# Optimization experiments

Hardware: AMD Instinct MI355X
Metric: run time of the kernel (lower is better)

Reference implementation:

```python
import jax, jax.numpy as jnp
import numpy as np

H = 16  # num_heads

def _toroidal_bias(S, dtype):
    # float mask: +1.0 at (i, (i-1)%S), (i,i), (i, (i+1)%S); PyTorch ADDS float attn_mask to scores
    eye = jnp.eye(S, dtype=dtype)
    return eye + jnp.roll(eye, 1, axis=1) + jnp.roll(eye, -1, axis=1)

def setup_inputs() -> dict:
    key = jax.random.key(0)
    ks = jax.random.split(key, 7)
    E = 1024
    S, B = 2048, 2
    sc = 0.02
    return {
        "x": jax.random.normal(ks[0], (S, B, E), dtype=jnp.float32),
        "w_tor": jax.random.normal(ks[1], (E, E), dtype=jnp.float32) * sc,
        "b_tor": jax.random.normal(ks[2], (E,), dtype=jnp.float32) * sc,
        "in_proj_w": jax.random.normal(ks[3], (3 * E, E), dtype=jnp.float32) * sc,
        "in_proj_b": jax.random.normal(ks[4], (3 * E,), dtype=jnp.float32) * sc,
        "out_w": jax.random.normal(ks[5], (E, E), dtype=jnp.float32) * sc,
        "out_b": jax.random.normal(ks[6], (E,), dtype=jnp.float32) * sc,
    }

def reference(x, w_tor, b_tor, in_proj_w, in_proj_b, out_w, out_b):
    S, B, E = x.shape
    hd = E // H
    scale = 1.0 / jnp.sqrt(jnp.asarray(hd, dtype=x.dtype))
    # toroidal projection, then fused in_proj (self-attention: q=k=v=x_toroidal)
    xt = x @ w_tor.T + b_tor                      # (S,B,E)
    qkv = xt @ in_proj_w.T + in_proj_b            # (S,B,3E)
    q, k, v = jnp.split(qkv, 3, axis=-1)
    def to_heads(t):
        return t.reshape(S, B, H, hd).transpose(1, 2, 0, 3)  # (B,H,S,hd)
    q, k, v = to_heads(q), to_heads(k), to_heads(v)
    bias = _toroidal_bias(S, x.dtype)             # (S,S) additive float mask
    scores = jnp.einsum('bhqd,bhkd->bhqk', q * scale, k) + bias
    attn = jax.nn.softmax(scores, axis=-1)
    o = jnp.einsum('bhqk,bhkd->bhqd', attn, v)    # (B,H,S,hd)
    o = o.transpose(2, 0, 1, 3).reshape(S, B, E)
    return o @ out_w.T + out_b
```

## Files before the change

### kernel.cpp

```cpp
#include <hip/hip_runtime.h>

#define S_LEN 2048
#define NB    2
#define EMB   1024
#define NH    16
#define HD    64

typedef __bf16 bf16_t;
typedef bf16_t bf16x8 __attribute__((ext_vector_type(8)));
typedef bf16_t bf16x4v __attribute__((ext_vector_type(4)));
typedef float  f32x4  __attribute__((ext_vector_type(4)));

#define L2E 1.44269504f

__device__ __forceinline__ void g2l16(const void* g, void* l) {
    auto gp = reinterpret_cast<const unsigned int __attribute__((address_space(1)))*>(
        reinterpret_cast<uintptr_t>(g));
    auto lp = reinterpret_cast<unsigned int __attribute__((address_space(3)))*>(
        reinterpret_cast<uintptr_t>(l));
    __builtin_amdgcn_global_load_lds(gp, lp, 16, 0, 0);
}

__global__ __launch_bounds__(256) void cast4_f32_bf16(
    const float* __restrict__ s0, bf16_t* __restrict__ d0,
    const float* __restrict__ s1, bf16_t* __restrict__ d1,
    const float* __restrict__ s2, bf16_t* __restrict__ d2,
    const float* __restrict__ s3, bf16_t* __restrict__ d3)
{
    long i = (long)blockIdx.x * 256 + threadIdx.x;
    const float* s; bf16_t* d; long off;
    if (i < 1048576)      { s = s0; d = d0; off = i; }
    else if (i < 1310720) { s = s1; d = d1; off = i - 1048576; }
    else if (i < 2097152) { s = s2; d = d2; off = i - 1310720; }
    else                  { s = s3; d = d3; off = i - 2097152; }
    float4 v = ((const float4*)s)[off];
    bf16x4v o;
    o[0] = (bf16_t)v.x; o[1] = (bf16_t)v.y; o[2] = (bf16_t)v.z; o[3] = (bf16_t)v.w;
    *(bf16x4v*)(d + off * 4) = o;
}

template<int TN, int MODE>
__global__ __launch_bounds__(256) void gemm_bt_bf16(
    const bf16_t* __restrict__ A, const bf16_t* __restrict__ W,
    const float* __restrict__ bias, void* __restrict__ Cout,
    bf16_t* __restrict__ Qp, bf16_t* __restrict__ Kp, bf16_t* __restrict__ Vp,
    int M, int N, int K)
{
    constexpr int MB = (TN == 128) ? 4 : 2;
    __shared__ __align__(16) bf16_t As[2][128 * 32];
    __shared__ __align__(16) bf16_t Bs[2][TN * 32];

    const int tid  = threadIdx.x;
    const int lane = tid & 63;
    const int w    = tid >> 6;
    const int lm   = lane & 15;
    const int lq   = lane >> 4;
    const long m0  = (long)blockIdx.y * 128;
    const long n0  = (long)blockIdx.x * TN;
    const int wm0  = (TN == 128) ? (w >> 1) * 64 : w * 32;
    const int wn0  = (TN == 128) ? (w & 1) * 64 : 0;

    f32x4 acc[MB][4];
#pragma unroll
    for (int i = 0; i < MB; ++i)
#pragma unroll
        for (int j = 0; j < 4; ++j) acc[i][j] = (f32x4){0.f, 0.f, 0.f, 0.f};

    auto stage = [&](int k0, int buf) {
        bf16_t* asb = &As[buf][0];
        bf16_t* bsb = &Bs[buf][0];
#pragma unroll
        for (int j = 0; j < 2; ++j) {
            int a   = (w * 2 + j) * 64 + lane;
            int row = a >> 2;
            int c   = (a & 3) ^ ((row >> 1) & 3);
            g2l16(A + (m0 + row) * K + k0 + c * 8, asb + (w * 2 + j) * 512);
        }
#pragma unroll
        for (int j = 0; j < TN / 64; ++j) {
            int a   = (w * (TN / 64) + j) * 64 + lane;
            int row = a >> 2;
            int c   = (a & 3) ^ ((row >> 1) & 3);
            g2l16(W + (n0 + row) * K + k0 + c * 8, bsb + (w * (TN / 64) + j) * 512);
        }
    };

    stage(0, 0);
    for (int k0 = 0; k0 < K; k0 += 32) {
        const int cur = (k0 >> 5) & 1;
        asm volatile("s_waitcnt vmcnt(0)" ::: "memory");
        __syncthreads();
        if (k0 + 32 < K) stage(k0 + 32, cur ^ 1);

        bf16x8 af[MB], bfr[4];
#pragma unroll
        for (int mb = 0; mb < MB; ++mb) {
            int r = wm0 + mb * 16 + lm;
            af[mb] = *(const bf16x8*)&As[cur][r * 32 + ((lq ^ ((r >> 1) & 3)) << 3)];
        }
#pragma unroll
        for (int nb = 0; nb < 4; ++nb) {
            int r = wn0 + nb * 16 + lm;
            bfr[nb] = *(const bf16x8*)&Bs[cur][r * 32 + ((lq ^ ((r >> 1) & 3)) << 3)];
        }
#pragma unroll
        for (int mb = 0; mb < MB; ++mb)
#pragma unroll
            for (int nb = 0; nb < 4; ++nb)
                acc[mb][nb] = __builtin_amdgcn_mfma_f32_16x16x32_bf16(
                    af[mb], bfr[nb], acc[mb][nb], 0, 0, 0);
    }

    float b4[4];
#pragma unroll
    for (int nb = 0; nb < 4; ++nb) b4[nb] = bias[n0 + wn0 + nb * 16 + lm];

#pragma unroll
    for (int mb = 0; mb < MB; ++mb) {
#pragma unroll
        for (int r = 0; r < 4; ++r) {
            long m = m0 + wm0 + mb * 16 + lq * 4 + r;
#pragma unroll
            for (int nb = 0; nb < 4; ++nb) {
                int n   = (int)n0 + wn0 + nb * 16 + lm;
                float v = acc[mb][nb][r] + b4[nb];
                if (MODE == 0) {
                    ((float*)Cout)[m * N + n] = v;
                } else if (MODE == 1) {
                    ((bf16_t*)Cout)[m * N + n] = (bf16_t)v;
                } else {
                    int sec  = n >> 10;
                    int nloc = n & 1023;
                    int h    = nloc >> 6;
                    int d    = nloc & 63;
                    bf16_t* dst = (sec == 0) ? Qp : (sec == 1 ? Kp : Vp);
                    float qs = (sec == 0) ? (0.125f * L2E) : 1.0f;
                    int s = (int)(m >> 1), b = (int)(m & 1);
                    dst[((size_t)((b * 16 + h) * S_LEN + s)) * 64 + d] = (bf16_t)(v * qs);
                }
            }
        }
    }
}

__global__ __launch_bounds__(256) void vtranspose(
    const bf16_t* __restrict__ Vb, bf16_t* __restrict__ Vtb)
{
    __shared__ bf16_t T[64][72];
    const int tid = threadIdx.x;
    const int bh  = blockIdx.x >> 5;
    const int st  = blockIdx.x & 31;
#pragma unroll
    for (int i = 0; i < 2; ++i) {
        int idx = i * 256 + tid;
        int r   = idx >> 3;
        int ch  = idx & 7;
        bf16x8 v = *(const bf16x8*)(Vb + ((size_t)(bh * S_LEN + st * 64 + r)) * 64 + ch * 8);
#pragma unroll
        for (int j = 0; j < 8; ++j) T[r][ch * 8 + j] = v[j];
    }
    __syncthreads();
#pragma unroll
    for (int i = 0; i < 2; ++i) {
        int idx = i * 256 + tid;
        int dd  = idx >> 3;
        int sc  = idx & 7;
        bf16x8 o;
#pragma unroll
        for (int j = 0; j < 8; ++j) o[j] = T[sc * 8 + j][dd];
        *(bf16x8*)(Vtb + ((size_t)(bh * 64 + dd)) * S_LEN + st * 64 + sc * 8) = o;
    }
}

__global__ __launch_bounds__(256) void attn_mfma(
    const bf16_t* __restrict__ Qb, const bf16_t* __restrict__ Kb,
    const bf16_t* __restrict__ Vtb, bf16_t* __restrict__ O)
{
    __shared__ __align__(16) bf16_t Ks[2][64 * 64];
    __shared__ __align__(16) bf16_t Vts[2][64 * 64];
    __shared__ __align__(16) bf16_t Ps[4][16 * 64];

    const int tid  = threadIdx.x;
    const int lane = tid & 63;
    const int w    = tid >> 6;
    const int bh   = blockIdx.x >> 5;
    const int qt   = blockIdx.x & 31;
    const int lm   = lane & 15;
    const int lq   = lane >> 4;
    const int sr   = lane >> 3;
    const int chunk = (lane & 7) ^ (sr & 7);

    const bf16_t* qbase = Qb + ((size_t)bh * S_LEN + qt * 64 + w * 16 + lm) * 64 + lq * 8;
    const bf16x8 qf0 = *(const bf16x8*)(qbase);
    const bf16x8 qf1 = *(const bf16x8*)(qbase + 32);

    f32x4 oacc[4];
#pragma unroll
    for (int i = 0; i < 4; ++i) oacc[i] = (f32x4){0.f, 0.f, 0.f, 0.f};
    float plsum[4] = {0.f, 0.f, 0.f, 0.f};

    bf16_t* psw = &Ps[w][0];

    auto stageKV = [&](int kt, int buf) {
        bf16_t* ksb = &Ks[buf][0];
        bf16_t* vsb = &Vts[buf][0];
        const bf16_t* kt_g = Kb + ((size_t)bh * S_LEN + kt * 64) * 64;
        g2l16(kt_g + (size_t)(w * 16 + sr) * 64 + chunk * 8,     ksb + (w * 16) * 64);
        g2l16(kt_g + (size_t)(w * 16 + 8 + sr) * 64 + chunk * 8, ksb + (w * 16 + 8) * 64);
        const bf16_t* vt_g = Vtb + (size_t)bh * 64 * S_LEN + kt * 64;
        g2l16(vt_g + (size_t)(w * 16 + sr) * S_LEN + chunk * 8,     vsb + (w * 16) * 64);
        g2l16(vt_g + (size_t)(w * 16 + 8 + sr) * S_LEN + chunk * 8, vsb + (w * 16 + 8) * 64);
    };

    stageKV(0, 0);
    for (int kt = 0; kt < 32; ++kt) {
        const int cur = kt & 1;
        asm volatile("s_waitcnt vmcnt(0)" ::: "memory");
        __syncthreads();
        if (kt < 31) stageKV(kt + 1, cur ^ 1);

        f32x4 S[4];
#pragma unroll
        for (int nb = 0; nb < 4; ++nb) {
            int key = nb * 16 + lm;
            bf16x8 kf0 = *(const bf16x8*)&Ks[cur][key * 64 + (((lq)     ^ (key & 7)) << 3)];
            bf16x8 kf1 = *(const bf16x8*)&Ks[cur][key * 64 + (((4 + lq) ^ (key & 7)) << 3)];
            f32x4 z = (f32x4){0.f, 0.f, 0.f, 0.f};
            z = __builtin_amdgcn_mfma_f32_16x16x32_bf16(qf0, kf0, z, 0, 0, 0);
            z = __builtin_amdgcn_mfma_f32_16x16x32_bf16(qf1, kf1, z, 0, 0, 0);
            S[nb] = z;
        }

        int ktd = (kt - qt) & 31;
        if (ktd <= 1 || ktd == 31) {
#pragma unroll
            for (int nb = 0; nb < 4; ++nb) {
                int key = kt * 64 + nb * 16 + lm;
#pragma unroll
                for (int r = 0; r < 4; ++r) {
                    int qrow = qt * 64 + w * 16 + lq * 4 + r;
                    int diff = (key - qrow) & (S_LEN - 1);
                    if (diff <= 1 || diff == S_LEN - 1) S[nb][r] += L2E;
                }
            }
        }

#pragma unroll
        for (int nb = 0; nb < 4; ++nb) {
            int colc = nb * 2 + (lm >> 3);
            int colw = lm & 7;
#pragma unroll
            for (int r = 0; r < 4; ++r) {
                float p = __builtin_amdgcn_exp2f(S[nb][r] - 12.0f);
                plsum[r] += p;
                int row = lq * 4 + r;
                psw[row * 64 + (((colc ^ (row & 7)) << 3) + colw)] = (bf16_t)p;
            }
        }

        bf16x8 pf0 = *(const bf16x8*)&psw[lm * 64 + (((lq)     ^ (lm & 7)) << 3)];
        bf16x8 pf1 = *(const bf16x8*)&psw[lm * 64 + (((4 + lq) ^ (lm & 7)) << 3)];

#pragma unroll
        for (int nbd = 0; nbd < 4; ++nbd) {
            int d = nbd * 16 + lm;
            bf16x8 vf0 = *(const bf16x8*)&Vts[cur][d * 64 + (((lq)     ^ (d & 7)) << 3)];
            bf16x8 vf1 = *(const bf16x8*)&Vts[cur][d * 64 + (((4 + lq) ^ (d & 7)) << 3)];
            oacc[nbd] = __builtin_amdgcn_mfma_f32_16x16x32_bf16(pf0, vf0, oacc[nbd], 0, 0, 0);
            oacc[nbd] = __builtin_amdgcn_mfma_f32_16x16x32_bf16(pf1, vf1, oacc[nbd], 0, 0, 0);
        }
    }

#pragma unroll
    for (int off = 1; off < 16; off <<= 1)
#pragma unroll
        for (int r = 0; r < 4; ++r)
            plsum[r] += __shfl_xor(plsum[r], off, 64);

    const int b = bh >> 4, h = bh & 15;
#pragma unroll
    for (int r = 0; r < 4; ++r) {
        float inv = 1.0f / plsum[r];
        int s = qt * 64 + w * 16 + lq * 4 + r;
        size_t rowbase = ((size_t)(s * NB + b)) * EMB + h * 64 + lm;
#pragma unroll
        for (int nbd = 0; nbd < 4; ++nbd)
            O[rowbase + nbd * 16] = (bf16_t)(oacc[nbd][r] * inv);
    }
}

extern "C" void kernel_launch(void* const* d_in, const int* in_sizes, int n_in,
                              void* d_out, int out_size, void* d_ws, size_t ws_size,
                              hipStream_t stream)
{
    const float* x         = (const float*)d_in[0];
    const float* w_tor     = (const float*)d_in[1];
    const float* b_tor     = (const float*)d_in[2];
    const float* in_proj_w = (const float*)d_in[3];
    const float* in_proj_b = (const float*)d_in[4];
    const float* out_w     = (const float*)d_in[5];
    const float* out_b     = (const float*)d_in[6];
    float* out = (float*)d_out;

    const int M = S_LEN * NB;

    char* base = (char*)d_ws;
    bf16_t* xb    = (bf16_t*)(base);
    bf16_t* wtorb = (bf16_t*)(base + ( 8ull << 20));
    bf16_t* ipwb  = (bf16_t*)(base + (10ull << 20));
    bf16_t* outwb = (bf16_t*)(base + (16ull << 20));
    bf16_t* xtb   = (bf16_t*)(base + (18ull << 20));
    bf16_t* Kb    = (bf16_t*)(base + (26ull << 20));
    bf16_t* Vb    = (bf16_t*)(base + (34ull << 20));
    bf16_t* Vtb   = (bf16_t*)(base + (42ull << 20));
    bf16_t* Qb    = xb;
    bf16_t* Ob    = xtb;

    cast4_f32_bf16<<<dim3(9216), 256, 0, stream>>>(
        x, xb, w_tor, wtorb, in_proj_w, ipwb, out_w, outwb);

    gemm_bt_bf16<64, 1><<<dim3(EMB / 64, M / 128), 256, 0, stream>>>(
        xb, wtorb, b_tor, xtb, nullptr, nullptr, nullptr, M, EMB, EMB);

    gemm_bt_bf16<128, 2><<<dim3(3 * EMB / 128, M / 128), 256, 0, stream>>>(
        xtb, ipwb, in_proj_b, nullptr, Qb, Kb, Vb, M, 3 * EMB, EMB);

    vtranspose<<<dim3(32 * 32), 256, 0, stream>>>(Vb, Vtb);

    attn_mfma<<<dim3(32 * 32), 256, 0, stream>>>(Qb, Kb, Vtb, Ob);

    gemm_bt_bf16<64, 0><<<dim3(EMB / 64, M / 128), 256, 0, stream>>>(
        Ob, outwb, out_b, out, nullptr, nullptr, nullptr, M, EMB, EMB);
}
```

Baseline: 232.1 us.

## Fuse V transpose into QKV GEMM epilogue and pack P stores in attention

The QKV projection epilogue now writes V directly in transposed (head-dim-major) layout with a permuted key order inside each 64-key tile, so the separate vtranspose kernel and its intermediate buffer go away. The attention kernel writes P to LDS as packed 4-element vectors instead of scalar stores, relying on the permuted key order to keep the P·V product consistent. It also drops the constant -12 offset from the exp2, which removes an overflow guard and may risk overflow for larger scores. The transposed V stores in the GEMM epilogue are scattered 2-byte writes, which may cost more than the removed launch.

```diff
diff --git a/kernel.cpp b/kernel.cpp
--- a/kernel.cpp
+++ b/kernel.cpp
@@ -43,7 +43,7 @@
 __global__ __launch_bounds__(256) void gemm_bt_bf16(
     const bf16_t* __restrict__ A, const bf16_t* __restrict__ W,
     const float* __restrict__ bias, void* __restrict__ Cout,
-    bf16_t* __restrict__ Qp, bf16_t* __restrict__ Kp, bf16_t* __restrict__ Vp,
+    bf16_t* __restrict__ Qp, bf16_t* __restrict__ Kp, bf16_t* __restrict__ Vtp,
     int M, int N, int K)
 {
     constexpr int MB = (TN == 128) ? 4 : 2;
@@ -133,42 +133,22 @@
                     int nloc = n & 1023;
                     int h    = nloc >> 6;
                     int d    = nloc & 63;
-                    bf16_t* dst = (sec == 0) ? Qp : (sec == 1 ? Kp : Vp);
-                    float qs = (sec == 0) ? (0.125f * L2E) : 1.0f;
-                    int s = (int)(m >> 1), b = (int)(m & 1);
-                    dst[((size_t)((b * 16 + h) * S_LEN + s)) * 64 + d] = (bf16_t)(v * qs);
+                    int s    = (int)(m >> 1), b = (int)(m & 1);
+                    int bh   = b * 16 + h;
+                    if (sec == 0) {
+                        Qp[((size_t)(bh * S_LEN + s)) * 64 + d] =
+                            (bf16_t)(v * (0.125f * L2E));
+                    } else if (sec == 1) {
+                        Kp[((size_t)(bh * S_LEN + s)) * 64 + d] = (bf16_t)v;
+                    } else {
+                        int local = s & 63;
+                        int pos   = ((local & 15) << 2) | (local >> 4);
+                        Vtp[((size_t)(bh * 64 + d)) * S_LEN + (s & ~63) + pos] =
+                            (bf16_t)v;
+                    }
                 }
             }
         }
-    }
-}
-
-__global__ __launch_bounds__(256) void vtranspose(
-    const bf16_t* __restrict__ Vb, bf16_t* __restrict__ Vtb)
-{
-    __shared__ bf16_t T[64][72];
-    const int tid = threadIdx.x;
-    const int bh  = blockIdx.x >> 5;
-    const int st  = blockIdx.x & 31;
-#pragma unroll
-    for (int i = 0; i < 2; ++i) {
-        int idx = i * 256 + tid;
-        int r   = idx >> 3;
-        int ch  = idx & 7;
-        bf16x8 v = *(const bf16x8*)(Vb + ((size_t)(bh * S_LEN + st * 64 + r)) * 64 + ch * 8);
-#pragma unroll
-        for (int j = 0; j < 8; ++j) T[r][ch * 8 + j] = v[j];
-    }
-    __syncthreads();
-#pragma unroll
-    for (int i = 0; i < 2; ++i) {
-        int idx = i * 256 + tid;
-        int dd  = idx >> 3;
-        int sc  = idx & 7;
-        bf16x8 o;
-#pragma unroll
-        for (int j = 0; j < 8; ++j) o[j] = T[sc * 8 + j][dd];
-        *(bf16x8*)(Vtb + ((size_t)(bh * 64 + dd)) * S_LEN + st * 64 + sc * 8) = o;
     }
 }
 
@@ -246,20 +226,20 @@
         }
 
 #pragma unroll
-        for (int nb = 0; nb < 4; ++nb) {
-            int colc = nb * 2 + (lm >> 3);
-            int colw = lm & 7;
-#pragma unroll
-            for (int r = 0; r < 4; ++r) {
-                float p = __builtin_amdgcn_exp2f(S[nb][r] - 12.0f);
+        for (int r = 0; r < 4; ++r) {
+            int rowp = lq * 4 + r;
+            bf16x4v pk;
+#pragma unroll
+            for (int nb = 0; nb < 4; ++nb) {
+                float p = __builtin_amdgcn_exp2f(S[nb][r]);
                 plsum[r] += p;
-                int row = lq * 4 + r;
-                psw[row * 64 + (((colc ^ (row & 7)) << 3) + colw)] = (bf16_t)p;
+                pk[nb] = (bf16_t)p;
             }
-        }
-
-        bf16x8 pf0 = *(const bf16x8*)&psw[lm * 64 + (((lq)     ^ (lm & 7)) << 3)];
-        bf16x8 pf1 = *(const bf16x8*)&psw[lm * 64 + (((4 + lq) ^ (lm & 7)) << 3)];
+            *(bf16x4v*)&psw[rowp * 64 + (((lm >> 1) ^ (rowp & 7)) << 3) + ((lm & 1) << 2)] = pk;
+        }
+
+        bf16x8 pf0 = *(const bf16x8*)&psw[lm * 64 + ((lq       ^ (lm & 7)) << 3)];
+        bf16x8 pf1 = *(const bf16x8*)&psw[lm * 64 + (((4 | lq) ^ (lm & 7)) << 3)];
 
 #pragma unroll
         for (int nbd = 0; nbd < 4; ++nbd) {
@@ -311,8 +291,7 @@
     bf16_t* outwb = (bf16_t*)(base + (16ull << 20));
     bf16_t* xtb   = (bf16_t*)(base + (18ull << 20));
     bf16_t* Kb    = (bf16_t*)(base + (26ull << 20));
-    bf16_t* Vb    = (bf16_t*)(base + (34ull << 20));
-    bf16_t* Vtb   = (bf16_t*)(base + (42ull << 20));
+    bf16_t* Vtb   = (bf16_t*)(base + (34ull << 20));
     bf16_t* Qb    = xb;
     bf16_t* Ob    = xtb;
 
@@ -323,9 +302,7 @@
         xb, wtorb, b_tor, xtb, nullptr, nullptr, nullptr, M, EMB, EMB);
 
     gemm_bt_bf16<128, 2><<<dim3(3 * EMB / 128, M / 128), 256, 0, stream>>>(
-        xtb, ipwb, in_proj_b, nullptr, Qb, Kb, Vb, M, 3 * EMB, EMB);
-
-    vtranspose<<<dim3(32 * 32), 256, 0, stream>>>(Vb, Vtb);
+        xtb, ipwb, in_proj_b, nullptr, Qb, Kb, Vtb, M, 3 * EMB, EMB);
 
     attn_mfma<<<dim3(32 * 32), 256, 0, stream>>>(Qb, Kb, Vtb, Ob);
 
```

Result: faster. 226.2 us (-2.5%).
